# Performance work log

Hardware: AMD Instinct MI355X
Metric: run time of the kernel (lower is better)

The kernel has to match this reference:

```python
import jax, jax.numpy as jnp
import numpy as np

B, D, L = 32, 512, 4096   # batch, latent_dim (dim1), time length
N, D2 = 77, 768           # text tokens, text_latent_dim (dim2)
BC = 24                   # number of conditioned batch elements
H = 8                     # num_heads
EPS = 1e-5


def _layernorm(x, g, b):
    mu = jnp.mean(x, axis=-1, keepdims=True)
    var = jnp.mean(jnp.square(x - mu), axis=-1, keepdims=True)
    return (x - mu) * jax.lax.rsqrt(var + EPS) * g + b


def setup_inputs() -> dict:
    key = jax.random.key(0)
    ks = jax.random.split(key, 8)
    s = 0.02
    return {
        "input_tensor": jax.random.normal(ks[0], (B, D, L), jnp.float32),
        "condition_tensor": jax.random.normal(ks[1], (B, N, D2), jnp.float32),
        "cond_indices": jnp.arange(BC, dtype=jnp.int64 if jax.config.jax_enable_x64 else jnp.int32),
        "ln_g": jnp.ones((D,), jnp.float32),
        "ln_b": jnp.zeros((D,), jnp.float32),
        "tln_g": jnp.ones((D2,), jnp.float32),
        "tln_b": jnp.zeros((D2,), jnp.float32),
        "Wq": jax.random.normal(ks[2], (D, D), jnp.float32) * s,
        "bq": jnp.zeros((D,), jnp.float32),
        "Wk": jax.random.normal(ks[3], (D2, D), jnp.float32) * s,
        "bk": jnp.zeros((D,), jnp.float32),
        "Wv": jax.random.normal(ks[4], (D2, D), jnp.float32) * s,
        "bv": jnp.zeros((D,), jnp.float32),
    }


def reference(input_tensor, condition_tensor, cond_indices,
              ln_g, ln_b, tln_g, tln_b, Wq, bq, Wk, bk, Wv, bv):
    dh = D // H
    # gather conditioned rows; [Bc, D, L] -> [Bc, T=L, D]
    x_cond = jnp.transpose(input_tensor[cond_indices], (0, 2, 1))
    cond = condition_tensor[cond_indices]  # [Bc, N, D2]

    q = _layernorm(x_cond, ln_g, ln_b) @ Wq + bq           # [Bc, T, D]
    cn = _layernorm(cond, tln_g, tln_b)                     # [Bc, N, D2]
    k = (cn @ Wk + bk).reshape(BC, N, H, dh)
    v = (cn @ Wv + bv).reshape(BC, N, H, dh)

    q = jax.nn.softmax(q.reshape(BC, L, H, dh), axis=-1)   # feature-map softmax
    k = jax.nn.softmax(k, axis=1)                           # softmax over tokens N

    context = jnp.einsum('bnhk,bnhv->bhkv', k, v)           # [Bc, H, dh, dh]
    y = jnp.einsum('bthk,bhkv->bthv', q, context).reshape(BC, L, D)

    # scatter residual back: indices are unique, so .add == torch index assignment
    return input_tensor.at[cond_indices].add(jnp.transpose(y, (0, 2, 1)))
```

## Files before the change

### kernel.cpp

```cpp
#include <hip/hip_runtime.h>

#define LN_EPS 1e-5f

typedef __attribute__((ext_vector_type(8))) short bf16x8;
typedef __attribute__((ext_vector_type(4))) float f32x4;

__device__ __forceinline__ unsigned short f2bf(float f){
  unsigned u = __builtin_bit_cast(unsigned, f);
  u = (u + 0x7fffu + ((u >> 16) & 1u)) >> 16;
  return (unsigned short)u;
}
__device__ __forceinline__ float bf2f(unsigned short h){
  unsigned u = ((unsigned)h) << 16;
  return __builtin_bit_cast(float, u);
}
__device__ __forceinline__ void gll16(const void* g, void* l){
  __builtin_amdgcn_global_load_lds(
      (const __attribute__((address_space(1))) unsigned int*)(g),
      (__attribute__((address_space(3))) unsigned int*)(l), 16, 0, 0);
}

__global__ void k_prep(const float* __restrict__ Wq, const float* __restrict__ ln_g,
                       const float* __restrict__ ln_b, const float* __restrict__ bq,
                       unsigned short* __restrict__ gWqT, float2* __restrict__ c12)
{
  __shared__ float r1[64][4], r2[64][4];
  const int tid = threadIdx.x;
  const int n0 = blockIdx.x * 64;
  const int c = tid & 63, q = tid >> 6;
  const int n = n0 + c;
  const int swz = (n >> 1) & 3;
  float c1p = 0.f, c2p = 0.f;
  for(int i=0;i<128;i+=4){
    ushort4 pk;
    unsigned short* pp = (unsigned short*)&pk;
    #pragma unroll
    for(int j=0;j<4;j++){
      const int d = q*128 + i + j;
      const float wv = Wq[(size_t)d*512 + n];
      const unsigned short hb = f2bf(ln_g[d] * wv);
      pp[j] = hb;
      c2p += bf2f(hb);
      c1p += ln_b[d] * wv;
    }
    *(ushort4*)(gWqT + (size_t)n*512 + ((q*128 + i) ^ (swz << 3))) = pk;
  }
  r1[c][q] = c1p; r2[c][q] = c2p;
  __syncthreads();
  if(q == 0){
    float a = 0.f, b2 = 0.f;
    #pragma unroll
    for(int j=0;j<4;j++){ a += r1[c][j]; b2 += r2[c][j]; }
    c12[n] = make_float2(a + bq[n], b2);
  }
}

__global__ void k_condkv(const float* __restrict__ cond, const int* __restrict__ idx,
                         const float* __restrict__ tg, const float* __restrict__ tb,
                         const float* __restrict__ Wk, const float* __restrict__ bk,
                         const float* __restrict__ Wv, const float* __restrict__ bv,
                         float* __restrict__ kbuf, float* __restrict__ vbuf)
{
  __shared__ float cn[16][768];
  const int bc = blockIdx.z, nc = blockIdx.y, dc = blockIdx.x;
  const int b = idx[bc];
  const int n0 = nc * 16;
  int nrows = 77 - n0; if(nrows > 16) nrows = 16;
  const int w = threadIdx.x >> 6, lane = threadIdx.x & 63;

  for(int r = w; r < nrows; r += 4){
    const float* src = cond + ((size_t)b * 77 + n0 + r) * 768;
    float vals[12]; float s1 = 0.f, s2 = 0.f;
    #pragma unroll
    for(int i=0;i<12;i++){ float x = src[lane + i*64]; vals[i]=x; s1+=x; s2+=x*x; }
    #pragma unroll
    for(int off=1; off<64; off<<=1){ s1 += __shfl_xor(s1, off); s2 += __shfl_xor(s2, off); }
    const float mu  = s1 * (1.f/768.f);
    const float var = s2 * (1.f/768.f) - mu*mu;
    const float rs  = rsqrtf(var + LN_EPS);
    #pragma unroll
    for(int i=0;i<12;i++){ const int c2 = lane + i*64; cn[r][c2] = (vals[i]-mu)*rs*tg[c2] + tb[c2]; }
  }
  __syncthreads();

  const int dq = threadIdx.x & 63;
  const int part = threadIdx.x >> 6;
  const float* W    = (dc < 2) ? Wk : Wv;
  const float* bias = (dc < 2) ? bk : bv;
  float* obuf       = (dc < 2) ? kbuf : vbuf;
  const int d0 = (dc & 1) * 256 + dq * 4;

  float acc[4][4] = {};
  for(int i=0;i<768;i++){
    const float4 wv = *(const float4*)(W + (size_t)i * 512 + d0);
    #pragma unroll
    for(int j=0;j<4;j++){
      const float c = cn[part*4 + j][i];
      acc[j][0] += c * wv.x; acc[j][1] += c * wv.y;
      acc[j][2] += c * wv.z; acc[j][3] += c * wv.w;
    }
  }
  #pragma unroll
  for(int j=0;j<4;j++){
    const int r = part*4 + j, n = n0 + r;
    if(r < nrows){
      float4 o;
      o.x = acc[j][0] + bias[d0+0];
      o.y = acc[j][1] + bias[d0+1];
      o.z = acc[j][2] + bias[d0+2];
      o.w = acc[j][3] + bias[d0+3];
      *(float4*)(obuf + ((size_t)bc * 77 + n) * 512 + d0) = o;
    }
  }
}

__global__ void k_ctx(const float* __restrict__ kbuf, const float* __restrict__ vbuf,
                      unsigned short* __restrict__ ctxP)
{
  __shared__ float kk[77][64];
  __shared__ float vv[77][64];
  __shared__ float inv_s[64];
  const int h = blockIdx.x, bc = blockIdx.y;
  const int tid = threadIdx.x;
  for(int e = tid; e < 77*64; e += 256){
    const int n = e >> 6, c = e & 63;
    kk[n][c] = kbuf[((size_t)bc * 77 + n) * 512 + h*64 + c];
    vv[n][c] = vbuf[((size_t)bc * 77 + n) * 512 + h*64 + c];
  }
  __syncthreads();
  if(tid < 64){
    float m = -1e30f;
    for(int n=0;n<77;n++) m = fmaxf(m, kk[n][tid]);
    float s = 0.f;
    for(int n=0;n<77;n++){ const float e = __expf(kk[n][tid] - m); kk[n][tid] = e; s += e; }
    inv_s[tid] = 1.f / s;
  }
  __syncthreads();
  #pragma unroll
  for(int j=0;j<16;j++){
    const int o = tid + 256*j;
    const int v = o >> 6, k2 = o & 63;
    float a = 0.f;
    for(int n=0;n<77;n++) a += kk[n][k2] * vv[n][v];
    const int pos = ((((k2>>5)*4 + (v>>4))*4 + ((k2>>3)&3))*16 + (v&15))*8 + (k2&7);
    ctxP[((size_t)(bc*8 + h)) * 4096 + pos] = f2bf(a * inv_s[k2]);
  }
}

__global__ __launch_bounds__(256, 2)
void k_fused(const float* __restrict__ input, const int* __restrict__ idx,
             const unsigned short* __restrict__ gWqT, const float2* __restrict__ c12,
             const unsigned short* __restrict__ ctxP, float* __restrict__ out)
{
  const int ntile = blockIdx.x;
  const int mtile = blockIdx.y;
  const int tid = threadIdx.x;

  if(mtile >= 768){
    const int cid = (mtile - 768)*2 + ntile;
    const int nb = cid >> 6, chunk = cid & 63;
    int cnt = 0, bsel = 0;
    for(int b2 = 0; b2 < 32; ++b2){
      bool member = false;
      #pragma unroll
      for(int i2 = 0; i2 < 24; ++i2) member |= (idx[i2] == b2);
      if(!member){ if(cnt == nb) bsel = b2; ++cnt; }
    }
    const float4* s = (const float4*)(input + (size_t)bsel * 2097152) + chunk*8192;
    float4*       d = (float4*)      (out   + (size_t)bsel * 2097152) + chunk*8192;
    #pragma unroll
    for(int i = 0; i < 32; ++i) d[i*256 + tid] = s[i*256 + tid];
    return;
  }

  __shared__ __align__(16) char smem[50176];
  char* const Xb0 = smem;
  char* const Wb0 = smem + 8192;
  char* const Xb1 = smem + 24576;
  char* const Wb1 = smem + 32768;
  unsigned short* const P = (unsigned short*)smem;
  float* const mu_s = (float*)(smem + 49152);
  float* const rs_s = (float*)(smem + 49664);

  const int lane = tid & 63, w = tid >> 6;
  const int col = lane & 15, g = lane >> 4;
  const int wm = w >> 1, wn = w & 1;
  const int bc = mtile >> 5, b = idx[bc];
  const int t0 = (mtile & 31) * 128;
  const int nbase = ntile * 256;
  const float* xb = input + (size_t)b * 2097152;
  const char* wTb = (const char*)gWqT + (size_t)nbase * 1024;

  const int tq = tid >> 3;
  const int kb = tid & 7;
  const float* xsrc = xb + (size_t)(kb*4) * 4096 + t0 + tq*4;

  int wx[4];
  #pragma unroll
  for(int j=0;j<4;j++)
    wx[j] = (tq*4 + j)*64 + ((((kb>>1) ^ j) & 3) << 4) + ((kb & 1) << 3);

  int offA[4], offB[8];
  #pragma unroll
  for(int mt=0; mt<4; ++mt){
    const int rowA = wm*64 + mt*16 + col;
    offA[mt] = rowA*64 + ((g ^ (rowA & 3)) << 4);
  }
  #pragma unroll
  for(int nt=0; nt<8; ++nt){
    const int rowB = wn*128 + nt*16 + col;
    offB[nt] = rowB*64 + ((g ^ ((rowB >> 1) & 3)) << 4);
  }

  const int fW = tid * 16;

  #define STAGEW(ks, Wdst)                                                \
  { _Pragma("unroll")                                                     \
    for(int i=0;i<4;i++){                                                 \
      const int f = fW + i*4096;                                          \
      gll16(wTb + (size_t)(f>>6)*1024 + (ks)*64 + (f&63), (Wdst) + f);    \
    } }
  #define LOADX(xr, ks)                                                   \
  { _Pragma("unroll")                                                     \
    for(int j=0;j<4;j++) xr[j] = *(const float4*)(xsrc + (size_t)((ks)*32 + j) * 4096); }
  #define PUTX(xr, Xdst)                                                  \
  { *(ushort4*)((Xdst) + wx[0]) = make_ushort4(f2bf(xr[0].x), f2bf(xr[1].x), f2bf(xr[2].x), f2bf(xr[3].x)); \
    *(ushort4*)((Xdst) + wx[1]) = make_ushort4(f2bf(xr[0].y), f2bf(xr[1].y), f2bf(xr[2].y), f2bf(xr[3].y)); \
    *(ushort4*)((Xdst) + wx[2]) = make_ushort4(f2bf(xr[0].z), f2bf(xr[1].z), f2bf(xr[2].z), f2bf(xr[3].z)); \
    *(ushort4*)((Xdst) + wx[3]) = make_ushort4(f2bf(xr[0].w), f2bf(xr[1].w), f2bf(xr[2].w), f2bf(xr[3].w)); }
  #define STATS(xr)                                                       \
  { s1[0] += xr[0].x + xr[1].x + xr[2].x + xr[3].x;                       \
    s2[0] += xr[0].x*xr[0].x + xr[1].x*xr[1].x + xr[2].x*xr[2].x + xr[3].x*xr[3].x; \
    s1[1] += xr[0].y + xr[1].y + xr[2].y + xr[3].y;                       \
    s2[1] += xr[0].y*xr[0].y + xr[1].y*xr[1].y + xr[2].y*xr[2].y + xr[3].y*xr[3].y; \
    s1[2] += xr[0].z + xr[1].z + xr[2].z + xr[3].z;                       \
    s2[2] += xr[0].z*xr[0].z + xr[1].z*xr[1].z + xr[2].z*xr[2].z + xr[3].z*xr[3].z; \
    s1[3] += xr[0].w + xr[1].w + xr[2].w + xr[3].w;                       \
    s2[3] += xr[0].w*xr[0].w + xr[1].w*xr[1].w + xr[2].w*xr[2].w + xr[3].w*xr[3].w; }

  f32x4 acc[4][8] = {};
  float s1[4] = {0,0,0,0}, s2[4] = {0,0,0,0};

  {
    float4 xr[4];
    LOADX(xr, 0);
    STAGEW(0, Wb0);
    PUTX(xr, Xb0);
    STATS(xr);
  }
  __syncthreads();

  for(int ks = 0; ks < 16; ++ks){
    char* const Xc = (ks & 1) ? Xb1 : Xb0;
    char* const Wc = (ks & 1) ? Wb1 : Wb0;
    char* const Xn = (ks & 1) ? Xb0 : Xb1;
    char* const Wn = (ks & 1) ? Wb0 : Wb1;
    float4 xn[4];
    if(ks < 15){ LOADX(xn, ks+1); STAGEW(ks+1, Wn); }

    bf16x8 af[4], bfr[8];
    #pragma unroll
    for(int mt=0; mt<4; ++mt) af[mt]  = *(const bf16x8*)(Xc + offA[mt]);
    #pragma unroll
    for(int nt=0; nt<8; ++nt) bfr[nt] = *(const bf16x8*)(Wc + offB[nt]);
    #pragma unroll
    for(int mt=0; mt<4; ++mt)
      #pragma unroll
      for(int nt=0; nt<8; ++nt)
        acc[mt][nt] = __builtin_amdgcn_mfma_f32_16x16x32_bf16(af[mt], bfr[nt], acc[mt][nt], 0, 0, 0);

    if(ks < 15){ PUTX(xn, Xn); STATS(xn); }
    __syncthreads();
  }
  #undef STAGEW
  #undef LOADX
  #undef PUTX
  #undef STATS

  #pragma unroll
  for(int j=0;j<4;j++){
    #pragma unroll
    for(int off=1; off<8; off<<=1){
      s1[j] += __shfl_xor(s1[j], off);
      s2[j] += __shfl_xor(s2[j], off);
    }
  }
  if(kb == 0){
    #pragma unroll
    for(int j=0;j<4;j++){
      const int t = tq*4 + j;
      const float mu  = s1[j] * (1.f/512.f);
      const float var = s2[j] * (1.f/512.f) - mu*mu;
      mu_s[t] = mu;
      rs_s[t] = rsqrtf(var + LN_EPS);
    }
  }
  __syncthreads();

  float c1b[8], c2v[8];
  #pragma unroll
  for(int nt=0; nt<8; ++nt){
    const float2 cc = c12[nbase + wn*128 + nt*16 + col];
    c1b[nt] = cc.x;
    c2v[nt] = cc.y;
  }
  #pragma unroll
  for(int mt=0; mt<4; ++mt){
    #pragma unroll
    for(int r=0; r<4; ++r){
      const int tl = wm*64 + mt*16 + g*4 + r;
      const float rsr = rs_s[tl];
      const float mrc = rsr * mu_s[tl];
      float v[8];
      #pragma unroll
      for(int nt=0; nt<8; ++nt)
        v[nt] = rsr*acc[mt][nt][r] - mrc*c2v[nt] + c1b[nt];
      #pragma unroll
      for(int hh=0; hh<2; ++hh){
        float m = fmaxf(fmaxf(v[hh*4+0],v[hh*4+1]), fmaxf(v[hh*4+2],v[hh*4+3]));
        m = fmaxf(m, __shfl_xor(m, 1));
        m = fmaxf(m, __shfl_xor(m, 2));
        m = fmaxf(m, __shfl_xor(m, 4));
        m = fmaxf(m, __shfl_xor(m, 8));
        float s = 0.f;
        float e[4];
        #pragma unroll
        for(int q2=0;q2<4;++q2){ e[q2] = __expf(v[hh*4+q2] - m); s += e[q2]; }
        s += __shfl_xor(s, 1);
        s += __shfl_xor(s, 2);
        s += __shfl_xor(s, 4);
        s += __shfl_xor(s, 8);
        const float inv = 1.f / s;
        #pragma unroll
        for(int q2=0;q2<4;++q2) acc[mt][hh*4+q2][r] = e[q2] * inv;
      }
    }
  }

  unsigned short* const Pw = P + w * (64*72);
  float* const ob = out + (size_t)b * 2097152;
  #pragma unroll
  for(int hh=0; hh<2; ++hh){
    #pragma unroll
    for(int mt=0; mt<4; ++mt)
      #pragma unroll
      for(int ntl=0; ntl<4; ++ntl)
        #pragma unroll
        for(int r=0; r<4; ++r)
          Pw[(mt*16 + g*4 + r)*72 + ntl*16 + col] = f2bf(acc[mt][hh*4+ntl][r]);

    const int head = ntile*4 + wn*2 + hh;
    const unsigned short* cp = ctxP + (size_t)(bc*8 + head) * 4096;
    f32x4 y[4][4] = {};
    #pragma unroll
    for(int ks2=0; ks2<2; ++ks2){
      bf16x8 pa[4];
      #pragma unroll
      for(int mt=0; mt<4; ++mt)
        pa[mt] = *(const bf16x8*)(Pw + (mt*16 + col)*72 + ks2*32 + g*8);
      bf16x8 cv[4];
      #pragma unroll
      for(int vt=0; vt<4; ++vt)
        cv[vt] = *(const bf16x8*)(cp + (size_t)(((ks2*4 + vt)*4 + g)*16 + col) * 8);
      #pragma unroll
      for(int mt=0; mt<4; ++mt)
        #pragma unroll
        for(int vt=0; vt<4; ++vt)
          y[mt][vt] = __builtin_amdgcn_mfma_f32_16x16x32_bf16(pa[mt], cv[vt], y[mt][vt], 0, 0, 0);
    }
    #pragma unroll
    for(int mt=0; mt<4; ++mt)
      #pragma unroll
      for(int vt=0; vt<4; ++vt){
        const size_t a = (size_t)(head*64 + vt*16 + col)*4096
                       + (size_t)(t0 + wm*64 + mt*16 + g*4);
        const float4 xr4 = *(const float4*)(xb + a);
        float4 o4;
        o4.x = xr4.x + y[mt][vt][0];
        o4.y = xr4.y + y[mt][vt][1];
        o4.z = xr4.z + y[mt][vt][2];
        o4.w = xr4.w + y[mt][vt][3];
        *(float4*)(ob + a) = o4;
      }
  }
}

extern "C" void kernel_launch(void* const* d_in, const int* in_sizes, int n_in,
                              void* d_out, int out_size, void* d_ws, size_t ws_size,
                              hipStream_t stream)
{
  const float* input = (const float*)d_in[0];
  const float* cond  = (const float*)d_in[1];
  const int*   idx   = (const int*)d_in[2];
  const float* ln_g  = (const float*)d_in[3];
  const float* ln_b  = (const float*)d_in[4];
  const float* tln_g = (const float*)d_in[5];
  const float* tln_b = (const float*)d_in[6];
  const float* Wq    = (const float*)d_in[7];
  const float* bq    = (const float*)d_in[8];
  const float* Wk    = (const float*)d_in[9];
  const float* bk    = (const float*)d_in[10];
  const float* Wv    = (const float*)d_in[11];
  const float* bv    = (const float*)d_in[12];
  float* out = (float*)d_out;
  char*  ws  = (char*)d_ws;

  unsigned short* gWqT = (unsigned short*)(ws);
  float2*         c12  = (float2*)(ws + 524288);
  unsigned short* ctxP = (unsigned short*)(ws + 528384);
  float* kbuf = (float*)(ws + 2101248);
  float* vbuf = (float*)(ws + 2101248 + 3784704);

  k_prep  <<<dim3(8),       dim3(256), 0, stream>>>(Wq, ln_g, ln_b, bq, gWqT, c12);
  k_condkv<<<dim3(4,5,24),  dim3(256), 0, stream>>>(cond, idx, tln_g, tln_b, Wk, bk, Wv, bv, kbuf, vbuf);
  k_ctx   <<<dim3(8,24),    dim3(256), 0, stream>>>(kbuf, vbuf, ctxP);
  k_fused <<<dim3(2,1024),  dim3(256), 0, stream>>>(input, idx, gWqT, c12, ctxP, out);
}
```

Baseline: 427.6 us.

## Shrink fused GEMM tile to 64 rows, load Wq fragments directly from global

The fused kernel's M tile drops from 128 to 64 time steps, so twice as many blocks are launched, and each wave now owns one full head instead of a 2x2 wave split. Wq^T fragments are read straight from global memory into registers rather than staged through LDS with async global-to-LDS loads, which lets the kernel drop the swizzled weight layout and shrink shared memory. Occupancy is raised to 3 blocks per CU. LayerNorm statistics are reduced across waves through shared memory. In exchange, Wq is re-read from global/L2 per wave without LDS sharing, and the per-block reuse of X rows across the N dimension is lower.

Result: faster. 416.6 us (-2.6%).

```diff
diff --git a/kernel.cpp b/kernel.cpp
--- a/kernel.cpp
+++ b/kernel.cpp
@@ -13,11 +13,6 @@
 __device__ __forceinline__ float bf2f(unsigned short h){
   unsigned u = ((unsigned)h) << 16;
   return __builtin_bit_cast(float, u);
-}
-__device__ __forceinline__ void gll16(const void* g, void* l){
-  __builtin_amdgcn_global_load_lds(
-      (const __attribute__((address_space(1))) unsigned int*)(g),
-      (__attribute__((address_space(3))) unsigned int*)(l), 16, 0, 0);
 }
 
 __global__ void k_prep(const float* __restrict__ Wq, const float* __restrict__ ln_g,
@@ -29,7 +24,6 @@
   const int n0 = blockIdx.x * 64;
   const int c = tid & 63, q = tid >> 6;
   const int n = n0 + c;
-  const int swz = (n >> 1) & 3;
   float c1p = 0.f, c2p = 0.f;
   for(int i=0;i<128;i+=4){
     ushort4 pk;
@@ -43,7 +37,7 @@
       c2p += bf2f(hb);
       c1p += ln_b[d] * wv;
     }
-    *(ushort4*)(gWqT + (size_t)n*512 + ((q*128 + i) ^ (swz << 3))) = pk;
+    *(ushort4*)(gWqT + (size_t)n*512 + q*128 + i) = pk;
   }
   r1[c][q] = c1p; r2[c][q] = c2p;
   __syncthreads();
@@ -147,17 +141,17 @@
   }
 }
 
-__global__ __launch_bounds__(256, 2)
+__global__ __launch_bounds__(256, 3)
 void k_fused(const float* __restrict__ input, const int* __restrict__ idx,
              const unsigned short* __restrict__ gWqT, const float2* __restrict__ c12,
              const unsigned short* __restrict__ ctxP, float* __restrict__ out)
 {
-  const int ntile = blockIdx.x;
-  const int mtile = blockIdx.y;
+  const int nt  = blockIdx.x;
+  const int by  = blockIdx.y;
   const int tid = threadIdx.x;
 
-  if(mtile >= 768){
-    const int cid = (mtile - 768)*2 + ntile;
+  if(by >= 1536){
+    const int cid = (by - 1536)*2 + nt;
     const int nb = cid >> 6, chunk = cid & 63;
     int cnt = 0, bsel = 0;
     for(int b2 = 0; b2 < 32; ++b2){
@@ -173,216 +167,194 @@
     return;
   }
 
-  __shared__ __align__(16) char smem[50176];
-  char* const Xb0 = smem;
-  char* const Wb0 = smem + 8192;
-  char* const Xb1 = smem + 24576;
-  char* const Wb1 = smem + 32768;
+  __shared__ __align__(16) char smem[40960];
   unsigned short* const P = (unsigned short*)smem;
-  float* const mu_s = (float*)(smem + 49152);
-  float* const rs_s = (float*)(smem + 49664);
+  float* const mu_s = (float*)(smem + 37376);
+  float* const rs_s = (float*)(smem + 37632);
+  float* const red1 = (float*)(smem + 37888);
+  float* const red2 = (float*)(smem + 38912);
 
   const int lane = tid & 63, w = tid >> 6;
   const int col = lane & 15, g = lane >> 4;
-  const int wm = w >> 1, wn = w & 1;
-  const int bc = mtile >> 5, b = idx[bc];
-  const int t0 = (mtile & 31) * 128;
-  const int nbase = ntile * 256;
+  const int bc = by >> 6, b = idx[bc];
+  const int t0 = (by & 63) * 64;
+  const int nbase = nt * 256;
   const float* xb = input + (size_t)b * 2097152;
-  const char* wTb = (const char*)gWqT + (size_t)nbase * 1024;
-
-  const int tq = tid >> 3;
-  const int kb = tid & 7;
-  const float* xsrc = xb + (size_t)(kb*4) * 4096 + t0 + tq*4;
+
+  const int tq = tid & 15;
+  const int kb = tid >> 4;
+  const float* xsrc = xb + (size_t)(kb*2) * 4096 + t0 + tq*4;
 
   int wx[4];
   #pragma unroll
-  for(int j=0;j<4;j++)
-    wx[j] = (tq*4 + j)*64 + ((((kb>>1) ^ j) & 3) << 4) + ((kb & 1) << 3);
-
-  int offA[4], offB[8];
+  for(int j=0;j<4;j++){
+    const int t = tq*4 + j;
+    wx[j] = t*64 + ((((kb>>2) ^ ((t>>1)&3)) & 3) << 4) + ((kb & 3) << 2);
+  }
+  int offA[4];
   #pragma unroll
   for(int mt=0; mt<4; ++mt){
-    const int rowA = wm*64 + mt*16 + col;
-    offA[mt] = rowA*64 + ((g ^ (rowA & 3)) << 4);
-  }
-  #pragma unroll
-  for(int nt=0; nt<8; ++nt){
-    const int rowB = wn*128 + nt*16 + col;
-    offB[nt] = rowB*64 + ((g ^ ((rowB >> 1) & 3)) << 4);
-  }
-
-  const int fW = tid * 16;
-
-  #define STAGEW(ks, Wdst)                                                \
-  { _Pragma("unroll")                                                     \
-    for(int i=0;i<4;i++){                                                 \
-      const int f = fW + i*4096;                                          \
-      gll16(wTb + (size_t)(f>>6)*1024 + (ks)*64 + (f&63), (Wdst) + f);    \
-    } }
-  #define LOADX(xr, ks)                                                   \
-  { _Pragma("unroll")                                                     \
-    for(int j=0;j<4;j++) xr[j] = *(const float4*)(xsrc + (size_t)((ks)*32 + j) * 4096); }
-  #define PUTX(xr, Xdst)                                                  \
-  { *(ushort4*)((Xdst) + wx[0]) = make_ushort4(f2bf(xr[0].x), f2bf(xr[1].x), f2bf(xr[2].x), f2bf(xr[3].x)); \
-    *(ushort4*)((Xdst) + wx[1]) = make_ushort4(f2bf(xr[0].y), f2bf(xr[1].y), f2bf(xr[2].y), f2bf(xr[3].y)); \
-    *(ushort4*)((Xdst) + wx[2]) = make_ushort4(f2bf(xr[0].z), f2bf(xr[1].z), f2bf(xr[2].z), f2bf(xr[3].z)); \
-    *(ushort4*)((Xdst) + wx[3]) = make_ushort4(f2bf(xr[0].w), f2bf(xr[1].w), f2bf(xr[2].w), f2bf(xr[3].w)); }
-  #define STATS(xr)                                                       \
-  { s1[0] += xr[0].x + xr[1].x + xr[2].x + xr[3].x;                       \
-    s2[0] += xr[0].x*xr[0].x + xr[1].x*xr[1].x + xr[2].x*xr[2].x + xr[3].x*xr[3].x; \
-    s1[1] += xr[0].y + xr[1].y + xr[2].y + xr[3].y;                       \
-    s2[1] += xr[0].y*xr[0].y + xr[1].y*xr[1].y + xr[2].y*xr[2].y + xr[3].y*xr[3].y; \
-    s1[2] += xr[0].z + xr[1].z + xr[2].z + xr[3].z;                       \
-    s2[2] += xr[0].z*xr[0].z + xr[1].z*xr[1].z + xr[2].z*xr[2].z + xr[3].z*xr[3].z; \
-    s1[3] += xr[0].w + xr[1].w + xr[2].w + xr[3].w;                       \
-    s2[3] += xr[0].w*xr[0].w + xr[1].w*xr[1].w + xr[2].w*xr[2].w + xr[3].w*xr[3].w; }
-
-  f32x4 acc[4][8] = {};
+    const int row = mt*16 + col;
+    offA[mt] = row*64 + ((g ^ ((row>>1)&3)) << 4);
+  }
+  const char* wrow[4];
+  #pragma unroll
+  for(int ntl=0; ntl<4; ++ntl)
+    wrow[ntl] = (const char*)gWqT + (size_t)(nbase + w*64 + ntl*16 + col)*1024 + g*16;
+
+  #define PUTX(ya, yb2, Xd)                                           \
+  { _Pragma("unroll")                                                 \
+    for(int j=0;j<4;j++)                                              \
+      *(ushort2*)((Xd) + wx[j]) = make_ushort2(f2bf((&(ya).x)[j]), f2bf((&(yb2).x)[j])); }
+  #define STATS(ya, yb2)                                              \
+  { _Pragma("unroll")                                                 \
+    for(int j=0;j<4;j++){                                             \
+      const float a_ = (&(ya).x)[j], b_ = (&(yb2).x)[j];              \
+      s1[j] += a_ + b_; s2[j] += a_*a_ + b_*b_; } }
+
   float s1[4] = {0,0,0,0}, s2[4] = {0,0,0,0};
+  f32x4 acc[4][4] = {};
 
   {
-    float4 xr[4];
-    LOADX(xr, 0);
-    STAGEW(0, Wb0);
-    PUTX(xr, Xb0);
-    STATS(xr);
+    float4 xa  = *(const float4*)(xsrc);
+    float4 xb2 = *(const float4*)(xsrc + 4096);
+    STATS(xa, xb2);
+    PUTX(xa, xb2, smem);
   }
   __syncthreads();
 
   for(int ks = 0; ks < 16; ++ks){
-    char* const Xc = (ks & 1) ? Xb1 : Xb0;
-    char* const Wc = (ks & 1) ? Wb1 : Wb0;
-    char* const Xn = (ks & 1) ? Xb0 : Xb1;
-    char* const Wn = (ks & 1) ? Wb0 : Wb1;
-    float4 xn[4];
-    if(ks < 15){ LOADX(xn, ks+1); STAGEW(ks+1, Wn); }
-
-    bf16x8 af[4], bfr[8];
-    #pragma unroll
-    for(int mt=0; mt<4; ++mt) af[mt]  = *(const bf16x8*)(Xc + offA[mt]);
-    #pragma unroll
-    for(int nt=0; nt<8; ++nt) bfr[nt] = *(const bf16x8*)(Wc + offB[nt]);
+    char* const Xc = smem + ((ks & 1) << 12);
+    char* const Xn = smem + (((ks + 1) & 1) << 12);
+    float4 xa, xb2;
+    const bool pf = (ks < 15);
+    if(pf){
+      xa  = *(const float4*)(xsrc + (size_t)((ks+1)*32) * 4096);
+      xb2 = *(const float4*)(xsrc + (size_t)((ks+1)*32 + 1) * 4096);
+    }
+    bf16x8 bfr[4], af[4];
+    #pragma unroll
+    for(int ntl=0; ntl<4; ++ntl) bfr[ntl] = *(const bf16x8*)(wrow[ntl] + ks*64);
+    #pragma unroll
+    for(int mt=0; mt<4; ++mt) af[mt] = *(const bf16x8*)(Xc + offA[mt]);
     #pragma unroll
     for(int mt=0; mt<4; ++mt)
       #pragma unroll
-      for(int nt=0; nt<8; ++nt)
-        acc[mt][nt] = __builtin_amdgcn_mfma_f32_16x16x32_bf16(af[mt], bfr[nt], acc[mt][nt], 0, 0, 0);
-
-    if(ks < 15){ PUTX(xn, Xn); STATS(xn); }
+      for(int ntl=0; ntl<4; ++ntl)
+        acc[mt][ntl] = __builtin_amdgcn_mfma_f32_16x16x32_bf16(af[mt], bfr[ntl], acc[mt][ntl], 0, 0, 0);
+    if(pf){
+      STATS(xa, xb2);
+      PUTX(xa, xb2, Xn);
+    }
     __syncthreads();
   }
-  #undef STAGEW
-  #undef LOADX
   #undef PUTX
   #undef STATS
 
   #pragma unroll
   for(int j=0;j<4;j++){
-    #pragma unroll
-    for(int off=1; off<8; off<<=1){
-      s1[j] += __shfl_xor(s1[j], off);
-      s2[j] += __shfl_xor(s2[j], off);
-    }
-  }
-  if(kb == 0){
+    s1[j] += __shfl_xor(s1[j], 16); s2[j] += __shfl_xor(s2[j], 16);
+    s1[j] += __shfl_xor(s1[j], 32); s2[j] += __shfl_xor(s2[j], 32);
+  }
+  if(lane < 16){
     #pragma unroll
     for(int j=0;j<4;j++){
-      const int t = tq*4 + j;
-      const float mu  = s1[j] * (1.f/512.f);
-      const float var = s2[j] * (1.f/512.f) - mu*mu;
-      mu_s[t] = mu;
-      rs_s[t] = rsqrtf(var + LN_EPS);
-    }
-  }
-  __syncthreads();
-
-  float c1b[8], c2v[8];
-  #pragma unroll
-  for(int nt=0; nt<8; ++nt){
-    const float2 cc = c12[nbase + wn*128 + nt*16 + col];
-    c1b[nt] = cc.x;
-    c2v[nt] = cc.y;
+      red1[(lane*4 + j)*4 + w] = s1[j];
+      red2[(lane*4 + j)*4 + w] = s2[j];
+    }
+  }
+  __syncthreads();
+  if(tid < 64){
+    float a = 0.f, c = 0.f;
+    #pragma unroll
+    for(int ww=0; ww<4; ++ww){ a += red1[tid*4 + ww]; c += red2[tid*4 + ww]; }
+    const float mu  = a * (1.f/512.f);
+    const float var = c * (1.f/512.f) - mu*mu;
+    mu_s[tid] = mu;
+    rs_s[tid] = rsqrtf(var + LN_EPS);
+  }
+  __syncthreads();
+
+  const int head = nt*4 + w;
+  float c1b[4], c2v[4];
+  #pragma unroll
+  for(int ntl=0; ntl<4; ++ntl){
+    const float2 cc = c12[nbase + w*64 + ntl*16 + col];
+    c1b[ntl] = cc.x;
+    c2v[ntl] = cc.y;
   }
   #pragma unroll
   for(int mt=0; mt<4; ++mt){
     #pragma unroll
     for(int r=0; r<4; ++r){
-      const int tl = wm*64 + mt*16 + g*4 + r;
+      const int tl = mt*16 + g*4 + r;
       const float rsr = rs_s[tl];
       const float mrc = rsr * mu_s[tl];
-      float v[8];
-      #pragma unroll
-      for(int nt=0; nt<8; ++nt)
-        v[nt] = rsr*acc[mt][nt][r] - mrc*c2v[nt] + c1b[nt];
-      #pragma unroll
-      for(int hh=0; hh<2; ++hh){
-        float m = fmaxf(fmaxf(v[hh*4+0],v[hh*4+1]), fmaxf(v[hh*4+2],v[hh*4+3]));
-        m = fmaxf(m, __shfl_xor(m, 1));
-        m = fmaxf(m, __shfl_xor(m, 2));
-        m = fmaxf(m, __shfl_xor(m, 4));
-        m = fmaxf(m, __shfl_xor(m, 8));
-        float s = 0.f;
-        float e[4];
-        #pragma unroll
-        for(int q2=0;q2<4;++q2){ e[q2] = __expf(v[hh*4+q2] - m); s += e[q2]; }
-        s += __shfl_xor(s, 1);
-        s += __shfl_xor(s, 2);
-        s += __shfl_xor(s, 4);
-        s += __shfl_xor(s, 8);
-        const float inv = 1.f / s;
-        #pragma unroll
-        for(int q2=0;q2<4;++q2) acc[mt][hh*4+q2][r] = e[q2] * inv;
-      }
+      float v[4];
+      #pragma unroll
+      for(int ntl=0; ntl<4; ++ntl)
+        v[ntl] = rsr*acc[mt][ntl][r] - mrc*c2v[ntl] + c1b[ntl];
+      float m = fmaxf(fmaxf(v[0],v[1]), fmaxf(v[2],v[3]));
+      m = fmaxf(m, __shfl_xor(m, 1));
+      m = fmaxf(m, __shfl_xor(m, 2));
+      m = fmaxf(m, __shfl_xor(m, 4));
+      m = fmaxf(m, __shfl_xor(m, 8));
+      float s = 0.f;
+      #pragma unroll
+      for(int ntl=0; ntl<4; ++ntl){ v[ntl] = __expf(v[ntl] - m); s += v[ntl]; }
+      s += __shfl_xor(s, 1);
+      s += __shfl_xor(s, 2);
+      s += __shfl_xor(s, 4);
+      s += __shfl_xor(s, 8);
+      const float inv = 1.f / s;
+      #pragma unroll
+      for(int ntl=0; ntl<4; ++ntl) acc[mt][ntl][r] = v[ntl] * inv;
     }
   }
 
   unsigned short* const Pw = P + w * (64*72);
+  #pragma unroll
+  for(int mt=0; mt<4; ++mt)
+    #pragma unroll
+    for(int ntl=0; ntl<4; ++ntl)
+      #pragma unroll
+      for(int r=0; r<4; ++r)
+        Pw[(mt*16 + g*4 + r)*72 + ntl*16 + col] = f2bf(acc[mt][ntl][r]);
+
+  const unsigned short* cp = ctxP + (size_t)(bc*8 + head) * 4096;
+  f32x4 y[4][4] = {};
+  #pragma unroll
+  for(int ks2=0; ks2<2; ++ks2){
+    bf16x8 pa[4];
+    #pragma unroll
+    for(int mt=0; mt<4; ++mt)
+      pa[mt] = *(const bf16x8*)(Pw + (mt*16 + col)*72 + ks2*32 + g*8);
+    bf16x8 cv[4];
+    #pragma unroll
+    for(int vt=0; vt<4; ++vt)
+      cv[vt] = *(const bf16x8*)(cp + (size_t)(((ks2*4 + vt)*4 + g)*16 + col) * 8);
+    #pragma unroll
+    for(int mt=0; mt<4; ++mt)
+      #pragma unroll
+      for(int vt=0; vt<4; ++vt)
+        y[mt][vt] = __builtin_amdgcn_mfma_f32_16x16x32_bf16(pa[mt], cv[vt], y[mt][vt], 0, 0, 0);
+  }
+
   float* const ob = out + (size_t)b * 2097152;
   #pragma unroll
-  for(int hh=0; hh<2; ++hh){
-    #pragma unroll
-    for(int mt=0; mt<4; ++mt)
-      #pragma unroll
-      for(int ntl=0; ntl<4; ++ntl)
-        #pragma unroll
-        for(int r=0; r<4; ++r)
-          Pw[(mt*16 + g*4 + r)*72 + ntl*16 + col] = f2bf(acc[mt][hh*4+ntl][r]);
-
-    const int head = ntile*4 + wn*2 + hh;
-    const unsigned short* cp = ctxP + (size_t)(bc*8 + head) * 4096;
-    f32x4 y[4][4] = {};
-    #pragma unroll
-    for(int ks2=0; ks2<2; ++ks2){
-      bf16x8 pa[4];
-      #pragma unroll
-      for(int mt=0; mt<4; ++mt)
-        pa[mt] = *(const bf16x8*)(Pw + (mt*16 + col)*72 + ks2*32 + g*8);
-      bf16x8 cv[4];
-      #pragma unroll
-      for(int vt=0; vt<4; ++vt)
-        cv[vt] = *(const bf16x8*)(cp + (size_t)(((ks2*4 + vt)*4 + g)*16 + col) * 8);
-      #pragma unroll
-      for(int mt=0; mt<4; ++mt)
-        #pragma unroll
-        for(int vt=0; vt<4; ++vt)
-          y[mt][vt] = __builtin_amdgcn_mfma_f32_16x16x32_bf16(pa[mt], cv[vt], y[mt][vt], 0, 0, 0);
-    }
-    #pragma unroll
-    for(int mt=0; mt<4; ++mt)
-      #pragma unroll
-      for(int vt=0; vt<4; ++vt){
-        const size_t a = (size_t)(head*64 + vt*16 + col)*4096
-                       + (size_t)(t0 + wm*64 + mt*16 + g*4);
-        const float4 xr4 = *(const float4*)(xb + a);
-        float4 o4;
-        o4.x = xr4.x + y[mt][vt][0];
-        o4.y = xr4.y + y[mt][vt][1];
-        o4.z = xr4.z + y[mt][vt][2];
-        o4.w = xr4.w + y[mt][vt][3];
-        *(float4*)(ob + a) = o4;
-      }
-  }
+  for(int mt=0; mt<4; ++mt)
+    #pragma unroll
+    for(int vt=0; vt<4; ++vt){
+      const size_t a = (size_t)(head*64 + vt*16 + col)*4096
+                     + (size_t)(t0 + mt*16 + g*4);
+      const float4 xr4 = *(const float4*)(xb + a);
+      float4 o4;
+      o4.x = xr4.x + y[mt][vt][0];
+      o4.y = xr4.y + y[mt][vt][1];
+      o4.z = xr4.z + y[mt][vt][2];
+      o4.w = xr4.w + y[mt][vt][3];
+      *(float4*)(ob + a) = o4;
+    }
 }
 
 extern "C" void kernel_launch(void* const* d_in, const int* in_sizes, int n_in,
@@ -414,5 +386,5 @@
   k_prep  <<<dim3(8),       dim3(256), 0, stream>>>(Wq, ln_g, ln_b, bq, gWqT, c12);
   k_condkv<<<dim3(4,5,24),  dim3(256), 0, stream>>>(cond, idx, tln_g, tln_b, Wk, bk, Wv, bv, kbuf, vbuf);
   k_ctx   <<<dim3(8,24),    dim3(256), 0, stream>>>(kbuf, vbuf, ctxP);
-  k_fused <<<dim3(2,1024),  dim3(256), 0, stream>>>(input, idx, gWqT, c12, ctxP, out);
-}
+  k_fused <<<dim3(2,1792),  dim3(256), 0, stream>>>(input, idx, gWqT, c12, ctxP, out);
+}
```
